# Kernel optimization log

Measured on AMD Instinct MI355X. Metric: run time of the kernel, lower is better.

Reference implementation:

```python
import jax, jax.numpy as jnp
import numpy as np

RPN_BATCH = 256
ROI_BATCH = 128
IMG = 800.0


def _box_iou(a, b):
    # a: [N,4], b: [G,4] -> [N,G]
    lt = jnp.maximum(a[:, None, :2], b[None, :, :2])
    rb = jnp.minimum(a[:, None, 2:], b[None, :, 2:])
    wh = jnp.clip(rb - lt, 0.0)
    inter = wh[..., 0] * wh[..., 1]
    area_a = (a[:, 2] - a[:, 0]) * (a[:, 3] - a[:, 1])
    area_b = (b[:, 2] - b[:, 0]) * (b[:, 3] - b[:, 1])
    return inter / (area_a[:, None] + area_b[None, :] - inter + 1e-6)


def _encode(a, t):
    wa = a[:, 2] - a[:, 0]
    ha = a[:, 3] - a[:, 1]
    xa = a[:, 0] + 0.5 * wa
    ya = a[:, 1] + 0.5 * ha
    wt = t[:, 2] - t[:, 0]
    ht = t[:, 3] - t[:, 1]
    xt = t[:, 0] + 0.5 * wt
    yt = t[:, 1] + 0.5 * ht
    return jnp.stack(((xt - xa) / wa, (yt - ya) / ha,
                      jnp.log(wt / wa + 1e-6), jnp.log(ht / ha + 1e-6)), axis=1)


def _smooth_l1(x):
    ax = jnp.abs(x)
    return jnp.where(ax < 1.0, 0.5 * x * x, ax - 0.5)


def _rpn_loss_one(scores, deltas, anchors, gt):
    # scores [N,1], deltas [N,4], anchors [N,4], gt [G,4]
    ious = _box_iou(anchors, gt)                 # [N,G]
    max_iou = ious.max(axis=1)
    argmax = ious.argmax(axis=1)
    labels = jnp.full((anchors.shape[0],), -1.0, dtype=scores.dtype)
    labels = jnp.where(max_iou < 0.3, 0.0, labels)
    labels = jnp.where(max_iou > 0.7, 1.0, labels)
    labels = labels.at[jnp.argmax(ious, axis=0)].set(1.0)  # each gt's best anchor is positive
    # deterministic subsampling: keep first K in index order (replaces randperm)
    num_pos = RPN_BATCH // 2
    pos = labels == 1.0
    labels = jnp.where(pos & (jnp.cumsum(pos) > num_pos), -1.0, labels)
    n_pos = jnp.sum(labels == 1.0)
    neg = labels == 0.0
    labels = jnp.where(neg & (jnp.cumsum(neg) > (RPN_BATCH - n_pos)), -1.0, labels)
    mask = (labels != -1.0).astype(scores.dtype)
    logit = scores[:, 0]
    t = jnp.clip(labels, 0.0, 1.0)
    bce = jnp.maximum(logit, 0.0) - logit * t + jnp.log1p(jnp.exp(-jnp.abs(logit)))
    cls = jnp.sum(bce * mask) / jnp.maximum(jnp.sum(mask), 1.0)
    tgt = _encode(anchors, gt[argmax])
    posm = (labels == 1.0).astype(scores.dtype)
    n_posf = jnp.sum(posm)
    reg = jnp.where(n_posf > 0,
                    jnp.sum(_smooth_l1(deltas - tgt) * posm[:, None])
                    / jnp.maximum(n_posf * 4.0, 1.0),
                    0.0)
    return cls + reg


def _det_loss_one(cls_scores, bbox_deltas, proposals, gt, gt_labels):
    # cls_scores [P,C], bbox_deltas [P,4C], proposals [P,4], gt [G,4], gt_labels [G]
    P = proposals.shape[0]
    ious = _box_iou(proposals, gt)
    max_iou = ious.max(axis=1)
    argmax = ious.argmax(axis=1)
    assigned = jnp.where(max_iou >= 0.5, gt_labels[argmax], 0)
    num_pos = ROI_BATCH // 4
    pos = assigned > 0
    pos_rank = jnp.cumsum(pos) - 1
    neg_rank = jnp.cumsum(~pos) - 1
    idx = jnp.arange(P)
    # sort key: first up-to-num_pos positives (index order), then negatives,
    # excess positives pushed to the end -> first ROI_BATCH entries are the sample
    key = jnp.where(pos,
                    jnp.where(pos_rank < num_pos, pos_rank, 2 * P + idx),
                    P + neg_rank)
    sampled = jnp.argsort(key)[:ROI_BATCH]
    t_labels = assigned[sampled]
    matched = gt[argmax[sampled]]
    t_deltas = _encode(proposals[sampled], matched)
    logp = jax.nn.log_softmax(cls_scores[sampled], axis=-1)
    cls = -jnp.mean(jnp.take_along_axis(logp, t_labels[:, None], axis=1)[:, 0])
    pd = bbox_deltas[sampled].reshape(ROI_BATCH, -1, 4)
    preds = pd[jnp.arange(ROI_BATCH), t_labels]  # class-specific deltas
    posm = (t_labels > 0).astype(cls_scores.dtype)
    n_pos = jnp.sum(posm)
    reg = jnp.where(n_pos > 0,
                    jnp.sum(_smooth_l1(preds - t_deltas) * posm[:, None])
                    / jnp.maximum(n_pos * 4.0, 1.0),
                    0.0)
    return cls + reg


def _rand_boxes(k, prefix):
    k1, k2 = jax.random.split(k)
    xy = jax.random.uniform(k1, prefix + (2,)) * (IMG - 130.0)
    wh = jax.random.uniform(k2, prefix + (2,)) * 120.0 + 8.0
    return jnp.concatenate([xy, xy + wh], axis=-1)


def setup_inputs() -> dict:
    B, N, P, G, C = 4, 250000, 1000, 32, 81
    key = jax.random.key(0)
    ks = jax.random.split(key, 8)
    return {
        "rpn_scores": jax.random.normal(ks[0], (B, N, 1), dtype=jnp.float32),
        "rpn_deltas": jax.random.normal(ks[1], (B, N, 4), dtype=jnp.float32) * 0.1,
        "cls_scores": jax.random.normal(ks[2], (B * P, C), dtype=jnp.float32),
        "bbox_deltas": jax.random.normal(ks[3], (B * P, 4 * C), dtype=jnp.float32) * 0.1,
        "anchors": _rand_boxes(ks[4], (N,)),
        "proposals": _rand_boxes(ks[5], (B, P)),
        "gt_boxes": _rand_boxes(ks[6], (B, G)),
        "gt_labels": jax.random.randint(ks[7], (B, G), 1, C, dtype=jnp.int32),
    }


def reference(rpn_scores, rpn_deltas, cls_scores, bbox_deltas,
              anchors, proposals, gt_boxes, gt_labels):
    B, P, _ = proposals.shape
    C = cls_scores.shape[-1]
    cls_b = cls_scores.reshape(B, P, C)
    del_b = bbox_deltas.reshape(B, P, 4 * C)
    rpn = jax.vmap(lambda s, d, g: _rpn_loss_one(s, d, anchors, g))(
        rpn_scores, rpn_deltas, gt_boxes)
    det = jax.vmap(_det_loss_one)(cls_b, del_b, proposals, gt_boxes, gt_labels)
    return jnp.sum(rpn) + jnp.sum(det)
```

## Files before the change

kernel.cpp:

```cpp
#include <hip/hip_runtime.h>
#include <math.h>
#include <stdint.h>

#define B_ 4
#define N_ 250000
#define P_ 1000
#define G_ 32
#define C_ 81
#define RPN_BATCH 256
#define ROI_BATCH 128

#define ABLK 1024
#define NBA ((N_ + ABLK - 1) / ABLK)
#define DETB 4

__device__ __forceinline__ float iou_one(float a0, float a1, float a2, float a3,
                                         float areaA,
                                         float b0, float b1, float b2, float b3) {
    float ltx = fmaxf(a0, b0), lty = fmaxf(a1, b1);
    float rbx = fminf(a2, b2), rby = fminf(a3, b3);
    float w = fmaxf(rbx - ltx, 0.f), h = fmaxf(rby - lty, 0.f);
    float inter = w * h;
    float areaB = (b2 - b0) * (b3 - b1);
    return inter / (areaA + areaB - inter + 1e-6f);
}

__device__ __forceinline__ unsigned long long shfl_xor_u64(unsigned long long v, int m) {
    unsigned lo = (unsigned)v, hi = (unsigned)(v >> 32);
    lo = __shfl_xor(lo, m);
    hi = __shfl_xor(hi, m);
    return ((unsigned long long)hi << 32) | lo;
}

__device__ __forceinline__ float smooth_l1(float x) {
    float ax = fabsf(x);
    return (ax < 1.f) ? 0.5f * x * x : ax - 0.5f;
}

__global__ void __launch_bounds__(256, 4) rpn_assign_det(
        const float* __restrict__ anchors, const float* __restrict__ gt_boxes,
        const int* __restrict__ gt_labels, const float* __restrict__ proposals,
        const float* __restrict__ cls_scores, const float* __restrict__ bbox_deltas,
        int8_t* __restrict__ labels, int* __restrict__ posCnt, int* __restrict__ negCnt,
        unsigned long long* __restrict__ blockBest, float* __restrict__ detPart,
        float* __restrict__ out, int out_size) {
    int b = blockIdx.y, tid = threadIdx.x;
    int lane = tid & 63, wave = tid >> 6;

    if (blockIdx.x >= NBA) {
        int h = blockIdx.x - NBA;
        __shared__ float sgt[G_ * 4];
        __shared__ int sgl[G_];
        __shared__ short sassign[P_];
        __shared__ unsigned char sargm[P_];
        __shared__ int ssamp[ROI_BATCH];
        __shared__ int swd[4];
        __shared__ float sc[4], srg[4];
        if (tid < G_ * 4) sgt[tid] = gt_boxes[b * G_ * 4 + tid];
        if (tid < G_) sgl[tid] = gt_labels[b * G_ + tid];
        __syncthreads();

        int myPos = 0;
        int labj[4];
#pragma unroll
        for (int j = 0; j < 4; ++j) {
            int p = tid * 4 + j;
            int labp = 0, am = 0;
            if (p < P_) {
                float4 A = ((const float4*)proposals)[b * P_ + p];
                float areaA = (A.z - A.x) * (A.w - A.y);
                float best = -1.f;
#pragma unroll 8
                for (int g = 0; g < G_; ++g) {
                    float iou = iou_one(A.x, A.y, A.z, A.w, areaA,
                                        sgt[g * 4], sgt[g * 4 + 1], sgt[g * 4 + 2], sgt[g * 4 + 3]);
                    if (iou > best) { best = iou; am = g; }
                }
                labp = (best >= 0.5f) ? sgl[am] : 0;
                sassign[p] = (short)labp;
                sargm[p] = (unsigned char)am;
                labj[j] = labp;
                myPos += (labp > 0);
            } else {
                labj[j] = -1;
            }
        }

        int inc = myPos;
        for (int off = 1; off < 64; off <<= 1) {
            int v = __shfl_up(inc, off);
            if (lane >= off) inc += v;
        }
        if (lane == 63) swd[wave] = inc;
        __syncthreads();
        int basew = 0, total = 0;
        for (int w = 0; w < 4; ++w) { if (w < wave) basew += swd[w]; total += swd[w]; }
        int pp = basew + inc - myPos;
        int npos_kept = min(total, ROI_BATCH / 4);
        int nneg_total = P_ - total;
#pragma unroll
        for (int j = 0; j < 4; ++j) {
            int p = tid * 4 + j;
            if (labj[j] < 0) break;
            int slot;
            if (labj[j] > 0) {
                slot = (pp < ROI_BATCH / 4) ? pp : npos_kept + nneg_total + (pp - ROI_BATCH / 4);
                pp++;
            } else {
                slot = npos_kept + (p - pp);
            }
            if (slot < ROI_BATCH) ssamp[slot] = p;
        }
        int np_det = npos_kept + max(0, ROI_BATCH - npos_kept - nneg_total);
        __syncthreads();

        int rowBase = h * (ROI_BATCH / DETB) + wave * 8;
        float clsAcc = 0.f;
        for (int k = 0; k < 8; k += 2) {
            int s0 = ssamp[rowBase + k], s1 = ssamp[rowBase + k + 1];
            const float* r0 = cls_scores + ((size_t)(b * P_ + s0)) * C_;
            const float* r1 = cls_scores + ((size_t)(b * P_ + s1)) * C_;
            float a1 = r0[lane], b1 = r1[lane];
            float a2 = (lane < C_ - 64) ? r0[64 + lane] : -INFINITY;
            float b2 = (lane < C_ - 64) ? r1[64 + lane] : -INFINITY;
            float m0 = fmaxf(a1, a2), m1 = fmaxf(b1, b2);
            for (int mm = 32; mm >= 1; mm >>= 1) {
                m0 = fmaxf(m0, __shfl_xor(m0, mm));
                m1 = fmaxf(m1, __shfl_xor(m1, mm));
            }
            float e0 = expf(a1 - m0) + ((lane < C_ - 64) ? expf(a2 - m0) : 0.f);
            float e1 = expf(b1 - m1) + ((lane < C_ - 64) ? expf(b2 - m1) : 0.f);
            for (int mm = 32; mm >= 1; mm >>= 1) {
                e0 += __shfl_xor(e0, mm);
                e1 += __shfl_xor(e1, mm);
            }
            int t0 = sassign[s0], t1 = sassign[s1];
            int q0 = (t0 < 64) ? t0 : t0 - 64;
            int q1 = (t1 < 64) ? t1 : t1 - 64;
            float lo0 = __shfl(a1, q0), hi0 = __shfl(a2, q0);
            float lo1 = __shfl(b1, q1), hi1 = __shfl(b2, q1);
            float v0 = (t0 < 64) ? lo0 : hi0;
            float v1 = (t1 < 64) ? lo1 : hi1;
            if (lane == 0)
                clsAcc += -(v0 - m0 - logf(e0)) - (v1 - m1 - logf(e1));
        }

        float regAcc = 0.f;
        if (lane < 8) {
            int r = rowBase + lane;
            int s = ssamp[r];
            int t = sassign[s];
            if (t > 0) {
                int g = sargm[s];
                float4 A = ((const float4*)proposals)[b * P_ + s];
                float t0g = sgt[g * 4], t1g = sgt[g * 4 + 1];
                float t2g = sgt[g * 4 + 2], t3g = sgt[g * 4 + 3];
                float wa = A.z - A.x, ha = A.w - A.y;
                float xa = A.x + 0.5f * wa, ya = A.y + 0.5f * ha;
                float wt = t2g - t0g, ht = t3g - t1g;
                float xt = t0g + 0.5f * wt, yt = t1g + 0.5f * ht;
                const float4 pd = *(const float4*)(bbox_deltas +
                        ((size_t)(b * P_ + s)) * (4 * C_) + 4 * t);
                regAcc = smooth_l1(pd.x - (xt - xa) / wa) + smooth_l1(pd.y - (yt - ya) / ha) +
                         smooth_l1(pd.z - logf(wt / wa + 1e-6f)) +
                         smooth_l1(pd.w - logf(ht / ha + 1e-6f));
            }
        }
        for (int mm = 32; mm >= 1; mm >>= 1) regAcc += __shfl_xor(regAcc, mm);
        if (lane == 0) { sc[wave] = clsAcc; srg[wave] = regAcc; }
        __syncthreads();
        if (tid == 0) {
            float cp = sc[0] + sc[1] + sc[2] + sc[3];
            float rp = srg[0] + srg[1] + srg[2] + srg[3];
            detPart[b * DETB + h] = cp / (float)ROI_BATCH +
                ((np_det > 0) ? rp / fmaxf((float)np_det * 4.f, 1.f) : 0.f);
        }
        return;
    }

    __shared__ float4 sA[ABLK];
    __shared__ unsigned char sPart[4][ABLK];
    __shared__ int sCnt[8];

    int base = blockIdx.x * ABLK;

    if (blockIdx.x == 0 && b == 0) {
        for (int i = tid; i < out_size; i += 256) out[i] = 0.f;
    }

    for (int t = tid; t < ABLK; t += 256) {
        int ai = base + t;
        float4 v = make_float4(0.f, 0.f, 0.f, 0.f);
        if (ai < N_) v = ((const float4*)anchors)[ai];
        sA[t] = v;
    }
    __syncthreads();

    int waveu = __builtin_amdgcn_readfirstlane(wave);

    const float4* gt4 = (const float4*)gt_boxes + b * G_ + waveu * 8;
    float g0[8], g1[8], g2[8], g3[8], gae[8];
#pragma unroll
    for (int j = 0; j < 8; ++j) {
        float4 g = gt4[j];
        g0[j] = g.x; g1[j] = g.y; g2[j] = g.z; g3[j] = g.w;
        gae[j] = (g.z - g.x) * (g.w - g.y) + 1e-6f;
    }

    float bi[8], bd[8]; int bx[8];
#pragma unroll
    for (int j = 0; j < 8; ++j) { bi[j] = 0.f; bd[j] = 1.f; bx[j] = 0; }

    for (int k = 0; k < ABLK / 64; ++k) {
        int a = k * 64 + lane;
        float4 A = sA[a];
        float areaA = (A.z - A.x) * (A.w - A.y);
        int gidx = base + a;
        float acc03 = 1e30f, acc07 = 1e30f;
#pragma unroll
        for (int j = 0; j < 8; ++j) {
            float ltx = fmaxf(A.x, g0[j]), lty = fmaxf(A.y, g1[j]);
            float rbx = fminf(A.z, g2[j]), rby = fminf(A.w, g3[j]);
            float w = fmaxf(rbx - ltx, 0.f), h = fmaxf(rby - lty, 0.f);
            float inter = w * h;
            float d = (areaA + gae[j]) - inter;
            acc03 = fminf(acc03, fmaf(0.3f, d, -inter));
            acc07 = fminf(acc07, fmaf(0.7f, d, -inter));
            float p1 = inter * bd[j], p2 = bi[j] * d;
            if (p1 > p2) { bi[j] = inter; bd[j] = d; bx[j] = gidx; }
        }
        sPart[wave][a] = (unsigned char)(((acc07 < 0.f) ? 2 : 0) | ((acc03 > 0.f) ? 1 : 0));
    }

#pragma unroll
    for (int j = 0; j < 8; ++j) {
        float i_ = bi[j], d_ = bd[j]; int x_ = bx[j];
        for (int m = 32; m >= 1; m >>= 1) {
            float oi = __shfl_xor(i_, m), od = __shfl_xor(d_, m);
            int ox = __shfl_xor(x_, m);
            float pa = oi * d_, pb = i_ * od;
            bool take = (pa > pb) || (pa == pb && ox < x_);
            if (take) { i_ = oi; d_ = od; x_ = ox; }
        }
        if (lane == 0) {
            float iou = i_ / d_;
            unsigned long long pk =
                (((unsigned long long)__float_as_uint(iou)) << 32) |
                (unsigned)(0xFFFFFFFFu - (unsigned)x_);
            blockBest[((size_t)b * G_ + wave * 8 + j) * NBA + blockIdx.x] = pk;
        }
    }
    __syncthreads();

    unsigned u0 = ((const unsigned*)&sPart[0][0])[tid];
    unsigned u1 = ((const unsigned*)&sPart[1][0])[tid];
    unsigned u2 = ((const unsigned*)&sPart[2][0])[tid];
    unsigned u3 = ((const unsigned*)&sPart[3][0])[tid];
    unsigned andb = u0 & u1 & u2 & u3;
    unsigned orb  = u0 | u1 | u2 | u3;
    int gbase = base + tid * 4;
    unsigned outw = 0; int cp = 0, cn = 0;
#pragma unroll
    for (int j = 0; j < 4; ++j) {
        int above = (orb >> (8 * j + 1)) & 1;
        int below = (andb >> (8 * j)) & 1;
        int lab = above ? 1 : (below ? 0 : -1);
        if (gbase + j < N_) { cp += (lab == 1); cn += (lab == 0); }
        outw |= ((unsigned)(unsigned char)(char)lab) << (8 * j);
    }
    if (gbase < N_)
        ((unsigned*)labels)[(((size_t)b * N_ + base) >> 2) + tid] = outw;

    for (int m = 32; m >= 1; m >>= 1) { cp += __shfl_xor(cp, m); cn += __shfl_xor(cn, m); }
    if (lane == 0) { sCnt[wave] = cp; sCnt[4 + wave] = cn; }
    __syncthreads();
    if (tid == 0) {
        posCnt[b * NBA + blockIdx.x] = sCnt[0] + sCnt[1] + sCnt[2] + sCnt[3];
        negCnt[b * NBA + blockIdx.x] = sCnt[4] + sCnt[5] + sCnt[6] + sCnt[7];
    }
}

__global__ void __launch_bounds__(256) rpn_promote_scan(
        const unsigned long long* __restrict__ blockBest, int8_t* __restrict__ labels,
        int* __restrict__ posCnt, int* __restrict__ negCnt,
        int* __restrict__ totPos, int* __restrict__ totNeg) {
    int b = blockIdx.x, tid = threadIdx.x;
    __shared__ int sp[256], sn[256];
    __shared__ unsigned wIdx[G_];

    sp[tid] = (tid < NBA) ? posCnt[b * NBA + tid] : 0;
    sn[tid] = (tid < NBA) ? negCnt[b * NBA + tid] : 0;

    int g = tid >> 3, sub = tid & 7;
    unsigned long long v = 0;
    for (int j = sub; j < NBA; j += 8) {
        unsigned long long x = blockBest[((size_t)b * G_ + g) * NBA + j];
        if (x > v) v = x;
    }
    for (int m = 4; m >= 1; m >>= 1) {
        unsigned long long o = shfl_xor_u64(v, m);
        if (o > v) v = o;
    }
    if (sub == 0) wIdx[g] = 0xFFFFFFFFu - (unsigned)(v & 0xFFFFFFFFull);
    __syncthreads();
    if (tid < G_) {
        unsigned w = wIdx[tid];
        bool first = true;
        for (int j = 0; j < tid; ++j) if (wIdx[j] == w) first = false;
        if (first) {
            size_t li = (size_t)b * N_ + w;
            int8_t old = labels[li];
            labels[li] = 1;
            int blk = (int)(w / ABLK);
            if (old != 1) atomicAdd(&sp[blk], 1);
            if (old == 0) atomicAdd(&sn[blk], -1);
        }
    }
    __syncthreads();

    int vp = sp[tid], vn = sn[tid];
    for (int off = 1; off < 256; off <<= 1) {
        int tp = 0, tn = 0;
        if (tid >= off) { tp = sp[tid - off]; tn = sn[tid - off]; }
        __syncthreads();
        sp[tid] += tp; sn[tid] += tn;
        __syncthreads();
    }
    if (tid < NBA) {
        posCnt[b * NBA + tid] = sp[tid] - vp;
        negCnt[b * NBA + tid] = sn[tid] - vn;
    }
    if (tid == 0) { totPos[b] = sp[255]; totNeg[b] = sn[255]; }
}

__global__ void __launch_bounds__(256) rpn_sample(
        const int8_t* __restrict__ labels, const float* __restrict__ rpn_scores,
        const float* __restrict__ rpn_deltas, const float* __restrict__ anchors,
        const float* __restrict__ gt_boxes,
        const int* __restrict__ posBase, const int* __restrict__ negBase,
        const int* __restrict__ totPos, const int* __restrict__ totNeg,
        const float* __restrict__ detPart, float* __restrict__ out) {
    int b = blockIdx.y, tid = threadIdx.x;
    int base = blockIdx.x * ABLK;
    __shared__ float sg[G_ * 4];
    __shared__ int swP[4], swN[4];
    __shared__ float sred[8];
    if (tid < G_ * 4) sg[tid] = gt_boxes[b * G_ * 4 + tid];

    int gbase = base + tid * 4;
    unsigned word = 0xFFFFFFFFu;
    if (gbase < N_)
        word = ((const unsigned*)labels)[(((size_t)b * N_ + base) >> 2) + tid];
    int lab[4]; int cntP = 0, cntN = 0;
#pragma unroll
    for (int j = 0; j < 4; ++j) {
        lab[j] = (int)(char)((word >> (8 * j)) & 0xFF);
        cntP += (lab[j] == 1); cntN += (lab[j] == 0);
    }
    int lane = tid & 63, wave = tid >> 6;
    int ip = cntP, inn = cntN;
    for (int off = 1; off < 64; off <<= 1) {
        int vp = __shfl_up(ip, off), vn = __shfl_up(inn, off);
        if (lane >= off) { ip += vp; inn += vn; }
    }
    if (lane == 63) { swP[wave] = ip; swN[wave] = inn; }
    __syncthreads();
    int bP = 0, bN = 0;
    for (int w = 0; w < wave; ++w) { bP += swP[w]; bN += swN[w]; }
    int pP = posBase[b * NBA + blockIdx.x] + bP + ip - cntP;
    int pN = negBase[b * NBA + blockIdx.x] + bN + inn - cntN;

    int npos = min(totPos[b], RPN_BATCH / 2);
    int negQ = RPN_BATCH - npos;

    float bce = 0.f, regv = 0.f;
#pragma unroll
    for (int j = 0; j < 4; ++j) {
        int i = gbase + j;
        if (i >= N_) break;
        if (lab[j] == 1) {
            int r = pP++;
            if (r < RPN_BATCH / 2) {
                float l = rpn_scores[(size_t)b * N_ + i];
                bce += fmaxf(l, 0.f) - l + log1pf(expf(-fabsf(l)));
                float4 A = ((const float4*)anchors)[i];
                float areaA = (A.z - A.x) * (A.w - A.y);
                float best = -1.f; int am = 0;
                for (int g = 0; g < G_; ++g) {
                    float iou = iou_one(A.x, A.y, A.z, A.w, areaA,
                                        sg[g * 4], sg[g * 4 + 1], sg[g * 4 + 2], sg[g * 4 + 3]);
                    if (iou > best) { best = iou; am = g; }
                }
                float t0 = sg[am * 4], t1 = sg[am * 4 + 1], t2 = sg[am * 4 + 2], t3 = sg[am * 4 + 3];
                float wa = A.z - A.x, ha = A.w - A.y;
                float xa = A.x + 0.5f * wa, ya = A.y + 0.5f * ha;
                float wt = t2 - t0, ht = t3 - t1;
                float xt = t0 + 0.5f * wt, yt = t1 + 0.5f * ht;
                float4 D = ((const float4*)rpn_deltas)[(size_t)b * N_ + i];
                regv += smooth_l1(D.x - (xt - xa) / wa) + smooth_l1(D.y - (yt - ya) / ha) +
                        smooth_l1(D.z - logf(wt / wa + 1e-6f)) + smooth_l1(D.w - logf(ht / ha + 1e-6f));
            }
        } else if (lab[j] == 0) {
            int r = pN++;
            if (r < negQ) {
                float l = rpn_scores[(size_t)b * N_ + i];
                bce += fmaxf(l, 0.f) + log1pf(expf(-fabsf(l)));
            }
        }
    }
    for (int m = 32; m >= 1; m >>= 1) { bce += __shfl_xor(bce, m); regv += __shfl_xor(regv, m); }
    if (lane == 0) { sred[wave] = bce; sred[4 + wave] = regv; }
    __syncthreads();
    if (tid == 0) {
        float sb = sred[0] + sred[1] + sred[2] + sred[3];
        float sr = sred[4] + sred[5] + sred[6] + sred[7];
        int rnp = min(totPos[b], RPN_BATCH / 2);
        int kneg = min(totNeg[b], RPN_BATCH - rnp);
        float denomC = fmaxf((float)(rnp + kneg), 1.f);
        float contrib = sb / denomC +
                        ((rnp > 0) ? sr / fmaxf((float)rnp * 4.f, 1.f) : 0.f);
        if (blockIdx.x == 0)
            contrib += detPart[b * DETB + 0] + detPart[b * DETB + 1] +
                       detPart[b * DETB + 2] + detPart[b * DETB + 3];
        if (contrib != 0.f || blockIdx.x == 0) atomicAdd(out, contrib);
    }
}

extern "C" void kernel_launch(void* const* d_in, const int* in_sizes, int n_in,
                              void* d_out, int out_size, void* d_ws, size_t ws_size,
                              hipStream_t stream) {
    const float* rpn_scores  = (const float*)d_in[0];
    const float* rpn_deltas  = (const float*)d_in[1];
    const float* cls_scores  = (const float*)d_in[2];
    const float* bbox_deltas = (const float*)d_in[3];
    const float* anchors     = (const float*)d_in[4];
    const float* proposals   = (const float*)d_in[5];
    const float* gt_boxes    = (const float*)d_in[6];
    const int*   gt_labels   = (const int*)d_in[7];
    float* out = (float*)d_out;

    char* ws = (char*)d_ws;
    size_t off = 0;
    auto alloc = [&](size_t bytes) -> char* {
        size_t o = (off + 255) & ~(size_t)255;
        off = o + bytes;
        return ws + o;
    };
    int8_t* labels = (int8_t*)alloc((size_t)B_ * N_);
    unsigned long long* blockBest = (unsigned long long*)alloc((size_t)B_ * G_ * NBA * 8);
    int* posCnt = (int*)alloc((size_t)B_ * NBA * 4);
    int* negCnt = (int*)alloc((size_t)B_ * NBA * 4);
    int* totPos = (int*)alloc(B_ * 4);
    int* totNeg = (int*)alloc(B_ * 4);
    float* detPart = (float*)alloc(B_ * DETB * 4);

    rpn_assign_det<<<dim3(NBA + DETB, B_), 256, 0, stream>>>(
            anchors, gt_boxes, gt_labels, proposals, cls_scores, bbox_deltas,
            labels, posCnt, negCnt, blockBest, detPart, out, out_size);
    rpn_promote_scan<<<B_, 256, 0, stream>>>(blockBest, labels, posCnt, negCnt,
                                             totPos, totNeg);
    rpn_sample<<<dim3(NBA, B_), 256, 0, stream>>>(labels, rpn_scores, rpn_deltas,
                                                  anchors, gt_boxes, posCnt, negCnt,
                                                  totPos, totNeg, detPart, out);
}
```

Baseline: 141.6 us.

## Fuse promote/scan into sample kernel using atomicMax per-gt winners

```diff
diff --git a/kernel.cpp b/kernel.cpp
--- a/kernel.cpp
+++ b/kernel.cpp
@@ -25,13 +25,6 @@
     return inter / (areaA + areaB - inter + 1e-6f);
 }
 
-__device__ __forceinline__ unsigned long long shfl_xor_u64(unsigned long long v, int m) {
-    unsigned lo = (unsigned)v, hi = (unsigned)(v >> 32);
-    lo = __shfl_xor(lo, m);
-    hi = __shfl_xor(hi, m);
-    return ((unsigned long long)hi << 32) | lo;
-}
-
 __device__ __forceinline__ float smooth_l1(float x) {
     float ax = fabsf(x);
     return (ax < 1.f) ? 0.5f * x * x : ax - 0.5f;
@@ -42,7 +35,7 @@
         const int* __restrict__ gt_labels, const float* __restrict__ proposals,
         const float* __restrict__ cls_scores, const float* __restrict__ bbox_deltas,
         int8_t* __restrict__ labels, int* __restrict__ posCnt, int* __restrict__ negCnt,
-        unsigned long long* __restrict__ blockBest, float* __restrict__ detPart,
+        unsigned long long* __restrict__ gtWin, float* __restrict__ detPart,
         float* __restrict__ out, int out_size) {
     int b = blockIdx.y, tid = threadIdx.x;
     int lane = tid & 63, wave = tid >> 6;
@@ -247,7 +240,7 @@
             unsigned long long pk =
                 (((unsigned long long)__float_as_uint(iou)) << 32) |
                 (unsigned)(0xFFFFFFFFu - (unsigned)x_);
-            blockBest[((size_t)b * G_ + wave * 8 + j) * NBA + blockIdx.x] = pk;
+            atomicMax(&gtWin[(size_t)b * G_ + wave * 8 + j], pk);
         }
     }
     __syncthreads();
@@ -280,37 +273,37 @@
     }
 }
 
-__global__ void __launch_bounds__(256) rpn_promote_scan(
-        const unsigned long long* __restrict__ blockBest, int8_t* __restrict__ labels,
-        int* __restrict__ posCnt, int* __restrict__ negCnt,
-        int* __restrict__ totPos, int* __restrict__ totNeg) {
-    int b = blockIdx.x, tid = threadIdx.x;
+__global__ void __launch_bounds__(256) rpn_sample(
+        const int8_t* __restrict__ labels, const float* __restrict__ rpn_scores,
+        const float* __restrict__ rpn_deltas, const float* __restrict__ anchors,
+        const float* __restrict__ gt_boxes,
+        const int* __restrict__ posCnt, const int* __restrict__ negCnt,
+        const unsigned long long* __restrict__ gtWin,
+        const float* __restrict__ detPart, float* __restrict__ out) {
+    int b = blockIdx.y, tid = threadIdx.x;
+    int base = blockIdx.x * ABLK;
+    __shared__ float sg[G_ * 4];
     __shared__ int sp[256], sn[256];
-    __shared__ unsigned wIdx[G_];
-
+    __shared__ unsigned swin[G_];
+    __shared__ int sBase[6];
+    __shared__ int swP[4], swN[4];
+    __shared__ float sred[8];
+
+    if (tid < G_ * 4) sg[tid] = gt_boxes[b * G_ * 4 + tid];
+    if (tid < G_) {
+        unsigned long long v = gtWin[(size_t)b * G_ + tid];
+        swin[tid] = 0xFFFFFFFFu - (unsigned)(v & 0xFFFFFFFFull);
+    }
     sp[tid] = (tid < NBA) ? posCnt[b * NBA + tid] : 0;
     sn[tid] = (tid < NBA) ? negCnt[b * NBA + tid] : 0;
-
-    int g = tid >> 3, sub = tid & 7;
-    unsigned long long v = 0;
-    for (int j = sub; j < NBA; j += 8) {
-        unsigned long long x = blockBest[((size_t)b * G_ + g) * NBA + j];
-        if (x > v) v = x;
-    }
-    for (int m = 4; m >= 1; m >>= 1) {
-        unsigned long long o = shfl_xor_u64(v, m);
-        if (o > v) v = o;
-    }
-    if (sub == 0) wIdx[g] = 0xFFFFFFFFu - (unsigned)(v & 0xFFFFFFFFull);
-    __syncthreads();
+    __syncthreads();
+
     if (tid < G_) {
-        unsigned w = wIdx[tid];
+        unsigned w = swin[tid];
         bool first = true;
-        for (int j = 0; j < tid; ++j) if (wIdx[j] == w) first = false;
+        for (int j = 0; j < tid; ++j) if (swin[j] == w) first = false;
         if (first) {
-            size_t li = (size_t)b * N_ + w;
-            int8_t old = labels[li];
-            labels[li] = 1;
+            int8_t old = labels[(size_t)b * N_ + w];
             int blk = (int)(w / ABLK);
             if (old != 1) atomicAdd(&sp[blk], 1);
             if (old == 0) atomicAdd(&sn[blk], -1);
@@ -326,52 +319,49 @@
         sp[tid] += tp; sn[tid] += tn;
         __syncthreads();
     }
-    if (tid < NBA) {
-        posCnt[b * NBA + tid] = sp[tid] - vp;
-        negCnt[b * NBA + tid] = sn[tid] - vn;
-    }
-    if (tid == 0) { totPos[b] = sp[255]; totNeg[b] = sn[255]; }
-}
-
-__global__ void __launch_bounds__(256) rpn_sample(
-        const int8_t* __restrict__ labels, const float* __restrict__ rpn_scores,
-        const float* __restrict__ rpn_deltas, const float* __restrict__ anchors,
-        const float* __restrict__ gt_boxes,
-        const int* __restrict__ posBase, const int* __restrict__ negBase,
-        const int* __restrict__ totPos, const int* __restrict__ totNeg,
-        const float* __restrict__ detPart, float* __restrict__ out) {
-    int b = blockIdx.y, tid = threadIdx.x;
-    int base = blockIdx.x * ABLK;
-    __shared__ float sg[G_ * 4];
-    __shared__ int swP[4], swN[4];
-    __shared__ float sred[8];
-    if (tid < G_ * 4) sg[tid] = gt_boxes[b * G_ * 4 + tid];
+    if (tid == blockIdx.x) {
+        sBase[0] = sp[tid] - vp; sBase[1] = sn[tid] - vn;
+        sBase[4] = vp; sBase[5] = vn;
+    }
+    if (tid == 255) { sBase[2] = sp[255]; sBase[3] = sn[255]; }
+    __syncthreads();
+
+    int posB = sBase[0], negB = sBase[1], totP = sBase[2], totN = sBase[3];
+    int cPblk = sBase[4], cNblk = sBase[5];
+    int npos = min(totP, RPN_BATCH / 2);
+    int negQ = RPN_BATCH - npos;
+    bool active = (cPblk > 0 && posB < RPN_BATCH / 2) || (cNblk > 0 && negB < negQ);
+    if (!active && blockIdx.x != 0) return;
 
     int gbase = base + tid * 4;
     unsigned word = 0xFFFFFFFFu;
     if (gbase < N_)
         word = ((const unsigned*)labels)[(((size_t)b * N_ + base) >> 2) + tid];
-    int lab[4]; int cntP = 0, cntN = 0;
+    int lab[4];
+#pragma unroll
+    for (int j = 0; j < 4; ++j) lab[j] = (int)(char)((word >> (8 * j)) & 0xFF);
+    for (int g = 0; g < G_; ++g) {
+        int d = (int)swin[g] - gbase;
+        if (d >= 0 && d < 4) lab[d] = 1;
+    }
+    int cntP = 0, cntN = 0;
 #pragma unroll
     for (int j = 0; j < 4; ++j) {
-        lab[j] = (int)(char)((word >> (8 * j)) & 0xFF);
-        cntP += (lab[j] == 1); cntN += (lab[j] == 0);
-    }
+        if (gbase + j < N_) { cntP += (lab[j] == 1); cntN += (lab[j] == 0); }
+    }
+
     int lane = tid & 63, wave = tid >> 6;
     int ip = cntP, inn = cntN;
     for (int off = 1; off < 64; off <<= 1) {
-        int vp = __shfl_up(ip, off), vn = __shfl_up(inn, off);
-        if (lane >= off) { ip += vp; inn += vn; }
+        int vpp = __shfl_up(ip, off), vnn = __shfl_up(inn, off);
+        if (lane >= off) { ip += vpp; inn += vnn; }
     }
     if (lane == 63) { swP[wave] = ip; swN[wave] = inn; }
     __syncthreads();
     int bP = 0, bN = 0;
     for (int w = 0; w < wave; ++w) { bP += swP[w]; bN += swN[w]; }
-    int pP = posBase[b * NBA + blockIdx.x] + bP + ip - cntP;
-    int pN = negBase[b * NBA + blockIdx.x] + bN + inn - cntN;
-
-    int npos = min(totPos[b], RPN_BATCH / 2);
-    int negQ = RPN_BATCH - npos;
+    int pP = posB + bP + ip - cntP;
+    int pN = negB + bN + inn - cntN;
 
     float bce = 0.f, regv = 0.f;
 #pragma unroll
@@ -414,8 +404,8 @@
     if (tid == 0) {
         float sb = sred[0] + sred[1] + sred[2] + sred[3];
         float sr = sred[4] + sred[5] + sred[6] + sred[7];
-        int rnp = min(totPos[b], RPN_BATCH / 2);
-        int kneg = min(totNeg[b], RPN_BATCH - rnp);
+        int rnp = min(totP, RPN_BATCH / 2);
+        int kneg = min(totN, RPN_BATCH - rnp);
         float denomC = fmaxf((float)(rnp + kneg), 1.f);
         float contrib = sb / denomC +
                         ((rnp > 0) ? sr / fmaxf((float)rnp * 4.f, 1.f) : 0.f);
@@ -447,19 +437,16 @@
         return ws + o;
     };
     int8_t* labels = (int8_t*)alloc((size_t)B_ * N_);
-    unsigned long long* blockBest = (unsigned long long*)alloc((size_t)B_ * G_ * NBA * 8);
     int* posCnt = (int*)alloc((size_t)B_ * NBA * 4);
     int* negCnt = (int*)alloc((size_t)B_ * NBA * 4);
-    int* totPos = (int*)alloc(B_ * 4);
-    int* totNeg = (int*)alloc(B_ * 4);
+    unsigned long long* gtWin = (unsigned long long*)alloc(B_ * G_ * 8);
     float* detPart = (float*)alloc(B_ * DETB * 4);
 
+    hipMemsetAsync(gtWin, 0, B_ * G_ * 8, stream);
     rpn_assign_det<<<dim3(NBA + DETB, B_), 256, 0, stream>>>(
             anchors, gt_boxes, gt_labels, proposals, cls_scores, bbox_deltas,
-            labels, posCnt, negCnt, blockBest, detPart, out, out_size);
-    rpn_promote_scan<<<B_, 256, 0, stream>>>(blockBest, labels, posCnt, negCnt,
-                                             totPos, totNeg);
+            labels, posCnt, negCnt, gtWin, detPart, out, out_size);
     rpn_sample<<<dim3(NBA, B_), 256, 0, stream>>>(labels, rpn_scores, rpn_deltas,
                                                   anchors, gt_boxes, posCnt, negCnt,
-                                                  totPos, totNeg, detPart, out);
+                                                  gtWin, detPart, out);
 }
```

Measured after the change: 164.6 us. 16.2% more time.
